# Kernel tuning notes

Hardware: AMD Instinct MI355X
Metric: run time of the kernel (lower is better)

## Reference

```python
import jax, jax.numpy as jnp
import numpy as np


def setup_inputs() -> dict:
    key = jax.random.key(0)
    k1, k2, k3, k4 = jax.random.split(key, 4)
    B, I, O, N, T = 4096, 512, 64, 32, 4
    E = N * T
    x = jax.random.normal(k1, (B, I), dtype=jnp.float32)
    dst_state = jax.random.uniform(k2, (B, N), dtype=jnp.float32)
    type_state = jax.random.uniform(k3, (B, T), dtype=jnp.float32)
    # orthogonal init with gain=0.01 approximated by small random weights; bias=0
    W = jax.random.normal(k4, (E, I, O), dtype=jnp.float32) * 0.01
    b = jnp.zeros((E, O), dtype=jnp.float32)
    return {"x": x, "dst_state": dst_state, "type_state": type_state, "W": W, "b": b}


def reference(x, dst_state, type_state, W, b):
    # gating weights: outer product of dst_state [B,N] and type_state [B,T],
    # flattened to [B, E] with E = N*T (row-major, matching torch view)
    B = x.shape[0]
    g = (dst_state[:, :, None] * type_state[:, None, :]).reshape(B, -1)  # [B,E]
    # per-expert linear then gated sum over experts, fused via einsum
    logits = jnp.einsum("bi,eio,be->bo", x, W, g) + jnp.einsum("be,eo->bo", g, b)
    # torch.distributions.Categorical(logits=...) normalizes logits
    return jax.nn.log_softmax(logits, axis=-1)
```

## Files before the change

kernel.cpp:

```cpp
#include <hip/hip_runtime.h>
#include <hip/hip_bf16.h>

typedef __bf16 bf16x8 __attribute__((ext_vector_type(8)));
typedef float  f32x4  __attribute__((ext_vector_type(4)));

#define B_SZ 4096
#define I_SZ 512
#define O_SZ 64
#define E_SZ 128
#define BM   256
#define G_EXP 8
#define EG_N  16
#define MT_N  16

__global__ void prep_xg(const float* __restrict__ x, __bf16* __restrict__ xb,
                        const float* __restrict__ ds, const float* __restrict__ ts,
                        float* __restrict__ gT) {
  int i = blockIdx.x * 256 + threadIdx.x;
  float4 v = ((const float4*)x)[i];
  union { __bf16 h[4]; ushort4 u4; } pk;
  pk.h[0] = (__bf16)v.x; pk.h[1] = (__bf16)v.y;
  pk.h[2] = (__bf16)v.z; pk.h[3] = (__bf16)v.w;
  ((ushort4*)xb)[i] = pk.u4;
  int e = i >> 12, b = i & 4095;
  gT[i] = ds[b * 32 + (e >> 2)] * ts[b * 4 + (e & 3)];
}

__global__ void prep_w(const float* __restrict__ W, __bf16* __restrict__ wt) {
  __shared__ __bf16 tile[64][66];
  int e  = blockIdx.x >> 3;
  int it = blockIdx.x & 7;
  const float* src = W + (size_t)e * I_SZ * O_SZ + (size_t)it * 64 * O_SZ;
  #pragma unroll
  for (int s = 0; s < 16; ++s) {
    int idx = s * 256 + threadIdx.x;
    int r = idx >> 6, o = idx & 63;
    tile[o][r] = (__bf16)src[idx];
  }
  __syncthreads();
  __bf16* dst = wt + (size_t)e * O_SZ * I_SZ + it * 64;
  #pragma unroll
  for (int s = 0; s < 4; ++s) {
    int idx = s * 256 + threadIdx.x;
    int o = idx >> 4, c = (idx & 15) << 2;
    union { __bf16 h[4]; ushort4 u4; } q;
    q.h[0] = tile[o][c + 0]; q.h[1] = tile[o][c + 1];
    q.h[2] = tile[o][c + 2]; q.h[3] = tile[o][c + 3];
    *(ushort4*)&dst[(size_t)o * I_SZ + c] = q.u4;
  }
}

__global__ __launch_bounds__(512, 2)
void mtc_gemm(const __bf16* __restrict__ xb, const __bf16* __restrict__ wt,
              const float* __restrict__ gT, const float* __restrict__ bias,
              float* __restrict__ partials) {
  __shared__ __align__(16) __bf16 wsh[2][8][64 * 64];
  __shared__ float gsh[G_EXP][BM];
  __shared__ float bsh[G_EXP][O_SZ];

  const int tid  = threadIdx.x;
  const int wave = tid >> 6;
  const int lane = tid & 63;

  int bid = (int)blockIdx.x;
  bid = (bid & 7) * 32 + (bid >> 3);
  const int mtile = bid & 15;
  const int eg    = bid >> 4;
  const int row0  = mtile * BM;
  const int e0    = eg * G_EXP;

  auto stage = [&](int sbuf, int e) {
    const __bf16* wsrc = wt + (size_t)(e0 + e) * O_SZ * I_SZ;
    int o = tid >> 3, p = tid & 7;
    int sl = p ^ (o & 7);
    #pragma unroll
    for (int kc = 0; kc < 8; ++kc) {
      __builtin_amdgcn_global_load_lds(
          (const __attribute__((address_space(1))) void*)(wsrc + (size_t)o * I_SZ + kc * 64 + sl * 8),
          (__attribute__((address_space(3))) void*)(&wsh[sbuf][kc][wave * 512]),
          16, 0, 0);
    }
  };

  stage(0, 0);

  for (int idx = tid; idx < G_EXP * BM; idx += 512)
    gsh[idx >> 8][idx & 255] =
        gT[(size_t)(e0 + (idx >> 8)) * B_SZ + row0 + (idx & 255)];

  bsh[tid >> 6][tid & 63] = bias[(size_t)e0 * O_SZ + tid];

  bf16x8 af[2][16];
  {
    const __bf16* xr = xb + (size_t)(row0 + wave * 32 + (lane & 15)) * I_SZ
                          + (lane >> 4) * 8;
    #pragma unroll
    for (int mf = 0; mf < 2; ++mf)
      #pragma unroll
      for (int j = 0; j < 16; ++j)
        af[mf][j] = *(const bf16x8*)(xr + mf * 16 * I_SZ + j * 32);
  }

  __syncthreads();

  f32x4 logits[2][4] = {};
  int buf = 0;
  for (int e = 0; e < G_EXP; ++e) {
    if (e < G_EXP - 1) {
      stage(buf ^ 1, e + 1);
      asm volatile("s_waitcnt vmcnt(8)" ::: "memory");
    } else {
      asm volatile("s_waitcnt vmcnt(0)" ::: "memory");
    }
    __builtin_amdgcn_s_barrier();

    float bv[4];
    #pragma unroll
    for (int nf = 0; nf < 4; ++nf)
      bv[nf] = bsh[e][nf * 16 + (lane & 15)];
    f32x4 acc[2][4];
    #pragma unroll
    for (int mf = 0; mf < 2; ++mf)
      #pragma unroll
      for (int nf = 0; nf < 4; ++nf)
        acc[mf][nf] = (f32x4){bv[nf], bv[nf], bv[nf], bv[nf]};

    __builtin_amdgcn_s_setprio(1);
    #pragma unroll
    for (int j = 0; j < 16; ++j) {
      const __bf16* wb = &wsh[buf][j >> 1][0];
      bf16x8 bfr[4];
      #pragma unroll
      for (int nf = 0; nf < 4; ++nf) {
        int o  = nf * 16 + (lane & 15);
        int q  = (j & 1) * 4 + (lane >> 4);
        int ph = q ^ (o & 7);
        bfr[nf] = *(const bf16x8*)(wb + o * 64 + ph * 8);
      }
      #pragma unroll
      for (int nf = 0; nf < 4; ++nf)
        #pragma unroll
        for (int mf = 0; mf < 2; ++mf)
          acc[mf][nf] = __builtin_amdgcn_mfma_f32_16x16x32_bf16(
              af[mf][j], bfr[nf], acc[mf][nf], 0, 0, 0);
    }
    __builtin_amdgcn_s_setprio(0);

    f32x4 gq[2];
    #pragma unroll
    for (int mf = 0; mf < 2; ++mf)
      gq[mf] = *(const f32x4*)&gsh[e][wave * 32 + mf * 16 + (lane >> 4) * 4];
    #pragma unroll
    for (int mf = 0; mf < 2; ++mf)
      #pragma unroll
      for (int nf = 0; nf < 4; ++nf)
        #pragma unroll
        for (int rg = 0; rg < 4; ++rg)
          logits[mf][nf][rg] += gq[mf][rg] * acc[mf][nf][rg];

    __builtin_amdgcn_s_barrier();
    buf ^= 1;
  }

  float* pout = partials + (size_t)eg * B_SZ * O_SZ + (size_t)row0 * O_SZ;
  #pragma unroll
  for (int mf = 0; mf < 2; ++mf)
    #pragma unroll
    for (int nf = 0; nf < 4; ++nf)
      #pragma unroll
      for (int rg = 0; rg < 4; ++rg) {
        int r = wave * 32 + mf * 16 + ((lane >> 4) << 2) + rg;
        int o = nf * 16 + (lane & 15);
        pout[(size_t)r * O_SZ + o] = logits[mf][nf][rg];
      }
}

__global__ __launch_bounds__(256)
void mtc_reduce(const float* __restrict__ partials, float* __restrict__ out) {
  int wave = threadIdx.x >> 6, lane = threadIdx.x & 63;
  int r = blockIdx.x * 4 + wave;
  float s = 0.f;
  #pragma unroll
  for (int k = 0; k < EG_N; ++k)
    s += partials[(size_t)k * B_SZ * O_SZ + (size_t)r * O_SZ + lane];
  float m = s;
  #pragma unroll
  for (int off = 32; off; off >>= 1) m = fmaxf(m, __shfl_xor(m, off));
  float ex = expf(s - m), sum = ex;
  #pragma unroll
  for (int off = 32; off; off >>= 1) sum += __shfl_xor(sum, off);
  out[(size_t)r * O_SZ + lane] = s - m - logf(sum);
}

extern "C" void kernel_launch(void* const* d_in, const int* in_sizes, int n_in,
                              void* d_out, int out_size, void* d_ws, size_t ws_size,
                              hipStream_t stream) {
  const float* x    = (const float*)d_in[0];
  const float* ds   = (const float*)d_in[1];
  const float* ts   = (const float*)d_in[2];
  const float* W    = (const float*)d_in[3];
  const float* bias = (const float*)d_in[4];
  float* out = (float*)d_out;

  char* w = (char*)d_ws;
  __bf16* xb      = (__bf16*)(w);
  __bf16* wt      = (__bf16*)(w + (4ull  << 20));
  float*  gT      = (float*) (w + (12ull << 20));
  float*  parts   = (float*) (w + (14ull << 20));

  prep_xg   <<<2048, 256, 0, stream>>>(x, xb, ds, ts, gT);
  prep_w    <<<1024, 256, 0, stream>>>(W, wt);
  mtc_gemm  <<< 256, 512, 0, stream>>>(xb, wt, gT, bias, parts);
  mtc_reduce<<<1024, 256, 0, stream>>>(parts, out);
}
```

Baseline: 58.19 us.

## Split K across wave pairs to halve LDS B-fragment reads in MoE GEMM

```diff
diff --git a/kernel.cpp b/kernel.cpp
--- a/kernel.cpp
+++ b/kernel.cpp
@@ -61,6 +61,8 @@
   const int tid  = threadIdx.x;
   const int wave = tid >> 6;
   const int lane = tid & 63;
+  const int rg   = wave >> 1;
+  const int kh   = wave & 1;
 
   int bid = (int)blockIdx.x;
   bid = (bid & 7) * 32 + (bid >> 3);
@@ -77,7 +79,7 @@
     for (int kc = 0; kc < 8; ++kc) {
       __builtin_amdgcn_global_load_lds(
           (const __attribute__((address_space(1))) void*)(wsrc + (size_t)o * I_SZ + kc * 64 + sl * 8),
-          (__attribute__((address_space(3))) void*)(&wsh[sbuf][kc][wave * 512]),
+          (__attribute__((address_space(3))) void*)(&wsh[sbuf][kc][(tid >> 6) * 512]),
           16, 0, 0);
     }
   };
@@ -90,20 +92,20 @@
 
   bsh[tid >> 6][tid & 63] = bias[(size_t)e0 * O_SZ + tid];
 
-  bf16x8 af[2][16];
+  bf16x8 af[4][8];
   {
-    const __bf16* xr = xb + (size_t)(row0 + wave * 32 + (lane & 15)) * I_SZ
-                          + (lane >> 4) * 8;
-    #pragma unroll
-    for (int mf = 0; mf < 2; ++mf)
-      #pragma unroll
-      for (int j = 0; j < 16; ++j)
+    const __bf16* xr = xb + (size_t)(row0 + rg * 64 + (lane & 15)) * I_SZ
+                          + kh * 256 + (lane >> 4) * 8;
+    #pragma unroll
+    for (int mf = 0; mf < 4; ++mf)
+      #pragma unroll
+      for (int j = 0; j < 8; ++j)
         af[mf][j] = *(const bf16x8*)(xr + mf * 16 * I_SZ + j * 32);
   }
 
   __syncthreads();
 
-  f32x4 logits[2][4] = {};
+  f32x4 logits[4][4] = {};
   int buf = 0;
   for (int e = 0; e < G_EXP; ++e) {
     if (e < G_EXP - 1) {
@@ -114,65 +116,66 @@
     }
     __builtin_amdgcn_s_barrier();
 
-    float bv[4];
-    #pragma unroll
-    for (int nf = 0; nf < 4; ++nf)
-      bv[nf] = bsh[e][nf * 16 + (lane & 15)];
-    f32x4 acc[2][4];
-    #pragma unroll
-    for (int mf = 0; mf < 2; ++mf)
-      #pragma unroll
-      for (int nf = 0; nf < 4; ++nf)
-        acc[mf][nf] = (f32x4){bv[nf], bv[nf], bv[nf], bv[nf]};
-
-    __builtin_amdgcn_s_setprio(1);
-    #pragma unroll
-    for (int j = 0; j < 16; ++j) {
-      const __bf16* wb = &wsh[buf][j >> 1][0];
-      bf16x8 bfr[4];
-      #pragma unroll
-      for (int nf = 0; nf < 4; ++nf) {
+    #pragma unroll
+    for (int nf = 0; nf < 4; ++nf) {
+      float bv = kh ? 0.f : bsh[e][nf * 16 + (lane & 15)];
+      f32x4 acc[4];
+      #pragma unroll
+      for (int mf = 0; mf < 4; ++mf)
+        acc[mf] = (f32x4){bv, bv, bv, bv};
+
+      __builtin_amdgcn_s_setprio(1);
+      #pragma unroll
+      for (int j = 0; j < 8; ++j) {
+        const __bf16* wb = &wsh[buf][kh * 4 + (j >> 1)][0];
         int o  = nf * 16 + (lane & 15);
         int q  = (j & 1) * 4 + (lane >> 4);
         int ph = q ^ (o & 7);
-        bfr[nf] = *(const bf16x8*)(wb + o * 64 + ph * 8);
+        bf16x8 bfr = *(const bf16x8*)(wb + o * 64 + ph * 8);
+        #pragma unroll
+        for (int mf = 0; mf < 4; ++mf)
+          acc[mf] = __builtin_amdgcn_mfma_f32_16x16x32_bf16(
+              af[mf][j], bfr, acc[mf], 0, 0, 0);
       }
-      #pragma unroll
-      for (int nf = 0; nf < 4; ++nf)
+      __builtin_amdgcn_s_setprio(0);
+
+      #pragma unroll
+      for (int mf = 0; mf < 4; ++mf) {
+        f32x4 gq = *(const f32x4*)&gsh[e][rg * 64 + mf * 16 + (lane >> 4) * 4];
         #pragma unroll
-        for (int mf = 0; mf < 2; ++mf)
-          acc[mf][nf] = __builtin_amdgcn_mfma_f32_16x16x32_bf16(
-              af[mf][j], bfr[nf], acc[mf][nf], 0, 0, 0);
+        for (int rgi = 0; rgi < 4; ++rgi)
+          logits[mf][nf][rgi] += gq[rgi] * acc[mf][rgi];
+      }
     }
-    __builtin_amdgcn_s_setprio(0);
-
-    f32x4 gq[2];
-    #pragma unroll
-    for (int mf = 0; mf < 2; ++mf)
-      gq[mf] = *(const f32x4*)&gsh[e][wave * 32 + mf * 16 + (lane >> 4) * 4];
-    #pragma unroll
-    for (int mf = 0; mf < 2; ++mf)
-      #pragma unroll
-      for (int nf = 0; nf < 4; ++nf)
-        #pragma unroll
-        for (int rg = 0; rg < 4; ++rg)
-          logits[mf][nf][rg] += gq[mf][rg] * acc[mf][nf][rg];
 
     __builtin_amdgcn_s_barrier();
     buf ^= 1;
   }
 
-  float* pout = partials + (size_t)eg * B_SZ * O_SZ + (size_t)row0 * O_SZ;
-  #pragma unroll
-  for (int mf = 0; mf < 2; ++mf)
-    #pragma unroll
-    for (int nf = 0; nf < 4; ++nf)
-      #pragma unroll
-      for (int rg = 0; rg < 4; ++rg) {
-        int r = wave * 32 + mf * 16 + ((lane >> 4) << 2) + rg;
-        int o = nf * 16 + (lane & 15);
-        pout[(size_t)r * O_SZ + o] = logits[mf][nf][rg];
+  float* exch = (float*)&wsh[0][0][0];
+  if (kh) {
+    #pragma unroll
+    for (int mf = 0; mf < 4; ++mf)
+      #pragma unroll
+      for (int nf = 0; nf < 4; ++nf)
+        *(f32x4*)&exch[rg * 4096 + (mf * 4 + nf) * 256 + lane * 4] = logits[mf][nf];
+  }
+  __syncthreads();
+  if (!kh) {
+    float* pout = partials + (size_t)eg * B_SZ * O_SZ + (size_t)row0 * O_SZ;
+    #pragma unroll
+    for (int mf = 0; mf < 4; ++mf)
+      #pragma unroll
+      for (int nf = 0; nf < 4; ++nf) {
+        f32x4 other = *(const f32x4*)&exch[rg * 4096 + (mf * 4 + nf) * 256 + lane * 4];
+        #pragma unroll
+        for (int rgi = 0; rgi < 4; ++rgi) {
+          int r = rg * 64 + mf * 16 + ((lane >> 4) << 2) + rgi;
+          int o = nf * 16 + (lane & 15);
+          pout[(size_t)r * O_SZ + o] = logits[mf][nf][rgi] + other[rgi];
+        }
       }
+  }
 }
 
 __global__ __launch_bounds__(256)
```

Measured after the change: 124.0 us. 113% more time.

## Halve GEMM row tile and split K staging to double block count

Applied to the files above, without the earlier changes.

```diff
diff --git a/kernel.cpp b/kernel.cpp
--- a/kernel.cpp
+++ b/kernel.cpp
@@ -8,10 +8,10 @@
 #define I_SZ 512
 #define O_SZ 64
 #define E_SZ 128
-#define BM   256
+#define BM   128
 #define G_EXP 8
 #define EG_N  16
-#define MT_N  16
+#define MT_N  32
 
 __global__ void prep_xg(const float* __restrict__ x, __bf16* __restrict__ xb,
                         const float* __restrict__ ds, const float* __restrict__ ts,
@@ -50,11 +50,11 @@
   }
 }
 
-__global__ __launch_bounds__(512, 2)
+__global__ __launch_bounds__(256, 2)
 void mtc_gemm(const __bf16* __restrict__ xb, const __bf16* __restrict__ wt,
               const float* __restrict__ gT, const float* __restrict__ bias,
               float* __restrict__ partials) {
-  __shared__ __align__(16) __bf16 wsh[2][8][64 * 64];
+  __shared__ __align__(16) __bf16 wsh[2][4][64 * 64];
   __shared__ float gsh[G_EXP][BM];
   __shared__ float bsh[G_EXP][O_SZ];
 
@@ -63,32 +63,33 @@
   const int lane = tid & 63;
 
   int bid = (int)blockIdx.x;
-  bid = (bid & 7) * 32 + (bid >> 3);
-  const int mtile = bid & 15;
-  const int eg    = bid >> 4;
+  bid = (bid & 7) * 64 + (bid >> 3);
+  const int mtile = bid & 31;
+  const int eg    = bid >> 5;
   const int row0  = mtile * BM;
   const int e0    = eg * G_EXP;
 
-  auto stage = [&](int sbuf, int e) {
-    const __bf16* wsrc = wt + (size_t)(e0 + e) * O_SZ * I_SZ;
-    int o = tid >> 3, p = tid & 7;
-    int sl = p ^ (o & 7);
-    #pragma unroll
-    for (int kc = 0; kc < 8; ++kc) {
+  auto stage = [&](int sbuf, int e, int kh) {
+    const __bf16* wsrc = wt + (size_t)(e0 + e) * O_SZ * I_SZ + kh * 256;
+    #pragma unroll
+    for (int d = 0; d < 8; ++d) {
+      int o  = (d & 1) * 32 + (tid >> 3);
+      int sl = (tid & 7) ^ (o & 7);
       __builtin_amdgcn_global_load_lds(
-          (const __attribute__((address_space(1))) void*)(wsrc + (size_t)o * I_SZ + kc * 64 + sl * 8),
-          (__attribute__((address_space(3))) void*)(&wsh[sbuf][kc][wave * 512]),
+          (const __attribute__((address_space(1))) void*)(wsrc + (size_t)o * I_SZ + (d >> 1) * 64 + sl * 8),
+          (__attribute__((address_space(3))) void*)(&wsh[sbuf][d >> 1][(d & 1) * 2048 + tid * 8]),
           16, 0, 0);
     }
   };
 
-  stage(0, 0);
-
-  for (int idx = tid; idx < G_EXP * BM; idx += 512)
-    gsh[idx >> 8][idx & 255] =
-        gT[(size_t)(e0 + (idx >> 8)) * B_SZ + row0 + (idx & 255)];
-
-  bsh[tid >> 6][tid & 63] = bias[(size_t)e0 * O_SZ + tid];
+  stage(0, 0, 0);
+
+  for (int idx = tid; idx < G_EXP * BM; idx += 256)
+    gsh[idx >> 7][idx & 127] =
+        gT[(size_t)(e0 + (idx >> 7)) * B_SZ + row0 + (idx & 127)];
+
+  for (int idx = tid; idx < G_EXP * O_SZ; idx += 256)
+    bsh[idx >> 6][idx & 63] = bias[(size_t)e0 * O_SZ + idx];
 
   bf16x8 af[2][16];
   {
@@ -97,66 +98,72 @@
     #pragma unroll
     for (int mf = 0; mf < 2; ++mf)
       #pragma unroll
-      for (int j = 0; j < 16; ++j)
-        af[mf][j] = *(const bf16x8*)(xr + mf * 16 * I_SZ + j * 32);
+      for (int jg = 0; jg < 16; ++jg)
+        af[mf][jg] = *(const bf16x8*)(xr + mf * 16 * I_SZ + jg * 32);
   }
 
   __syncthreads();
 
   f32x4 logits[2][4] = {};
+  f32x4 acc[2][4];
   int buf = 0;
-  for (int e = 0; e < G_EXP; ++e) {
-    if (e < G_EXP - 1) {
-      stage(buf ^ 1, e + 1);
+  for (int ph = 0; ph < 2 * G_EXP; ++ph) {
+    const int e  = ph >> 1;
+    const int kh = ph & 1;
+    if (ph < 2 * G_EXP - 1) {
+      stage(buf ^ 1, (ph + 1) >> 1, (ph + 1) & 1);
       asm volatile("s_waitcnt vmcnt(8)" ::: "memory");
     } else {
       asm volatile("s_waitcnt vmcnt(0)" ::: "memory");
     }
     __builtin_amdgcn_s_barrier();
 
-    float bv[4];
-    #pragma unroll
-    for (int nf = 0; nf < 4; ++nf)
-      bv[nf] = bsh[e][nf * 16 + (lane & 15)];
-    f32x4 acc[2][4];
-    #pragma unroll
-    for (int mf = 0; mf < 2; ++mf)
+    if (!kh) {
+      float bv[4];
       #pragma unroll
       for (int nf = 0; nf < 4; ++nf)
-        acc[mf][nf] = (f32x4){bv[nf], bv[nf], bv[nf], bv[nf]};
+        bv[nf] = bsh[e][nf * 16 + (lane & 15)];
+      #pragma unroll
+      for (int mf = 0; mf < 2; ++mf)
+        #pragma unroll
+        for (int nf = 0; nf < 4; ++nf)
+          acc[mf][nf] = (f32x4){bv[nf], bv[nf], bv[nf], bv[nf]};
+    }
 
     __builtin_amdgcn_s_setprio(1);
     #pragma unroll
-    for (int j = 0; j < 16; ++j) {
+    for (int j = 0; j < 8; ++j) {
       const __bf16* wb = &wsh[buf][j >> 1][0];
       bf16x8 bfr[4];
       #pragma unroll
       for (int nf = 0; nf < 4; ++nf) {
         int o  = nf * 16 + (lane & 15);
         int q  = (j & 1) * 4 + (lane >> 4);
-        int ph = q ^ (o & 7);
-        bfr[nf] = *(const bf16x8*)(wb + o * 64 + ph * 8);
+        int phs = q ^ (o & 7);
+        bfr[nf] = *(const bf16x8*)(wb + o * 64 + phs * 8);
       }
       #pragma unroll
       for (int nf = 0; nf < 4; ++nf)
         #pragma unroll
         for (int mf = 0; mf < 2; ++mf)
           acc[mf][nf] = __builtin_amdgcn_mfma_f32_16x16x32_bf16(
-              af[mf][j], bfr[nf], acc[mf][nf], 0, 0, 0);
+              af[mf][kh * 8 + j], bfr[nf], acc[mf][nf], 0, 0, 0);
     }
     __builtin_amdgcn_s_setprio(0);
 
-    f32x4 gq[2];
-    #pragma unroll
-    for (int mf = 0; mf < 2; ++mf)
-      gq[mf] = *(const f32x4*)&gsh[e][wave * 32 + mf * 16 + (lane >> 4) * 4];
-    #pragma unroll
-    for (int mf = 0; mf < 2; ++mf)
-      #pragma unroll
-      for (int nf = 0; nf < 4; ++nf)
+    if (kh) {
+      f32x4 gq[2];
+      #pragma unroll
+      for (int mf = 0; mf < 2; ++mf)
+        gq[mf] = *(const f32x4*)&gsh[e][wave * 32 + mf * 16 + (lane >> 4) * 4];
+      #pragma unroll
+      for (int mf = 0; mf < 2; ++mf)
         #pragma unroll
-        for (int rg = 0; rg < 4; ++rg)
-          logits[mf][nf][rg] += gq[mf][rg] * acc[mf][nf][rg];
+        for (int nf = 0; nf < 4; ++nf)
+          #pragma unroll
+          for (int rg = 0; rg < 4; ++rg)
+            logits[mf][nf][rg] += gq[mf][rg] * acc[mf][nf][rg];
+    }
 
     __builtin_amdgcn_s_barrier();
     buf ^= 1;
@@ -210,6 +217,6 @@
 
   prep_xg   <<<2048, 256, 0, stream>>>(x, xb, ds, ts, gT);
   prep_w    <<<1024, 256, 0, stream>>>(W, wt);
-  mtc_gemm  <<< 256, 512, 0, stream>>>(xb, wt, gT, bias, parts);
+  mtc_gemm  <<< 512, 256, 0, stream>>>(xb, wt, gT, bias, parts);
   mtc_reduce<<<1024, 256, 0, stream>>>(parts, out);
 }
```

Result: slower. 117.5 us (+102.0%).

## Fuse x conversion and gate computation into GEMM; store partials in bf16

Applied to the files above, without the earlier changes.

```diff
diff --git a/kernel.cpp b/kernel.cpp
--- a/kernel.cpp
+++ b/kernel.cpp
@@ -13,19 +13,6 @@
 #define EG_N  16
 #define MT_N  16
 
-__global__ void prep_xg(const float* __restrict__ x, __bf16* __restrict__ xb,
-                        const float* __restrict__ ds, const float* __restrict__ ts,
-                        float* __restrict__ gT) {
-  int i = blockIdx.x * 256 + threadIdx.x;
-  float4 v = ((const float4*)x)[i];
-  union { __bf16 h[4]; ushort4 u4; } pk;
-  pk.h[0] = (__bf16)v.x; pk.h[1] = (__bf16)v.y;
-  pk.h[2] = (__bf16)v.z; pk.h[3] = (__bf16)v.w;
-  ((ushort4*)xb)[i] = pk.u4;
-  int e = i >> 12, b = i & 4095;
-  gT[i] = ds[b * 32 + (e >> 2)] * ts[b * 4 + (e & 3)];
-}
-
 __global__ void prep_w(const float* __restrict__ W, __bf16* __restrict__ wt) {
   __shared__ __bf16 tile[64][66];
   int e  = blockIdx.x >> 3;
@@ -51,9 +38,9 @@
 }
 
 __global__ __launch_bounds__(512, 2)
-void mtc_gemm(const __bf16* __restrict__ xb, const __bf16* __restrict__ wt,
-              const float* __restrict__ gT, const float* __restrict__ bias,
-              float* __restrict__ partials) {
+void mtc_gemm(const float* __restrict__ x, const __bf16* __restrict__ wt,
+              const float* __restrict__ ds, const float* __restrict__ ts,
+              const float* __restrict__ bias, __bf16* __restrict__ partials) {
   __shared__ __align__(16) __bf16 wsh[2][8][64 * 64];
   __shared__ float gsh[G_EXP][BM];
   __shared__ float bsh[G_EXP][O_SZ];
@@ -84,21 +71,31 @@
 
   stage(0, 0);
 
-  for (int idx = tid; idx < G_EXP * BM; idx += 512)
-    gsh[idx >> 8][idx & 255] =
-        gT[(size_t)(e0 + (idx >> 8)) * B_SZ + row0 + (idx & 255)];
+  for (int idx = tid; idx < G_EXP * BM; idx += 512) {
+    int k = idx >> 8, r = idx & 255;
+    gsh[k][r] = ds[(size_t)(row0 + r) * 32 + ((e0 + k) >> 2)]
+              * ts[(size_t)(row0 + r) * 4 + (k & 3)];
+  }
 
   bsh[tid >> 6][tid & 63] = bias[(size_t)e0 * O_SZ + tid];
 
   bf16x8 af[2][16];
   {
-    const __bf16* xr = xb + (size_t)(row0 + wave * 32 + (lane & 15)) * I_SZ
-                          + (lane >> 4) * 8;
-    #pragma unroll
-    for (int mf = 0; mf < 2; ++mf)
-      #pragma unroll
-      for (int j = 0; j < 16; ++j)
-        af[mf][j] = *(const bf16x8*)(xr + mf * 16 * I_SZ + j * 32);
+    const float* xr = x + (size_t)(row0 + wave * 32 + (lane & 15)) * I_SZ
+                        + (lane >> 4) * 8;
+    #pragma unroll
+    for (int mf = 0; mf < 2; ++mf)
+      #pragma unroll
+      for (int j = 0; j < 16; ++j) {
+        f32x4 a = *(const f32x4*)(xr + mf * 16 * I_SZ + j * 32);
+        f32x4 b = *(const f32x4*)(xr + mf * 16 * I_SZ + j * 32 + 4);
+        bf16x8 v;
+        v[0] = (__bf16)a[0]; v[1] = (__bf16)a[1];
+        v[2] = (__bf16)a[2]; v[3] = (__bf16)a[3];
+        v[4] = (__bf16)b[0]; v[5] = (__bf16)b[1];
+        v[6] = (__bf16)b[2]; v[7] = (__bf16)b[3];
+        af[mf][j] = v;
+      }
   }
 
   __syncthreads();
@@ -162,7 +159,7 @@
     buf ^= 1;
   }
 
-  float* pout = partials + (size_t)eg * B_SZ * O_SZ + (size_t)row0 * O_SZ;
+  __bf16* pout = partials + (size_t)eg * B_SZ * O_SZ + (size_t)row0 * O_SZ;
   #pragma unroll
   for (int mf = 0; mf < 2; ++mf)
     #pragma unroll
@@ -171,18 +168,18 @@
       for (int rg = 0; rg < 4; ++rg) {
         int r = wave * 32 + mf * 16 + ((lane >> 4) << 2) + rg;
         int o = nf * 16 + (lane & 15);
-        pout[(size_t)r * O_SZ + o] = logits[mf][nf][rg];
+        pout[(size_t)r * O_SZ + o] = (__bf16)logits[mf][nf][rg];
       }
 }
 
 __global__ __launch_bounds__(256)
-void mtc_reduce(const float* __restrict__ partials, float* __restrict__ out) {
+void mtc_reduce(const __bf16* __restrict__ partials, float* __restrict__ out) {
   int wave = threadIdx.x >> 6, lane = threadIdx.x & 63;
   int r = blockIdx.x * 4 + wave;
   float s = 0.f;
   #pragma unroll
   for (int k = 0; k < EG_N; ++k)
-    s += partials[(size_t)k * B_SZ * O_SZ + (size_t)r * O_SZ + lane];
+    s += (float)partials[(size_t)k * B_SZ * O_SZ + (size_t)r * O_SZ + lane];
   float m = s;
   #pragma unroll
   for (int off = 32; off; off >>= 1) m = fmaxf(m, __shfl_xor(m, off));
@@ -203,13 +200,10 @@
   float* out = (float*)d_out;
 
   char* w = (char*)d_ws;
-  __bf16* xb      = (__bf16*)(w);
-  __bf16* wt      = (__bf16*)(w + (4ull  << 20));
-  float*  gT      = (float*) (w + (12ull << 20));
-  float*  parts   = (float*) (w + (14ull << 20));
-
-  prep_xg   <<<2048, 256, 0, stream>>>(x, xb, ds, ts, gT);
+  __bf16* wt      = (__bf16*)(w);
+  __bf16* parts   = (__bf16*)(w + (8ull << 20));
+
   prep_w    <<<1024, 256, 0, stream>>>(W, wt);
-  mtc_gemm  <<< 256, 512, 0, stream>>>(xb, wt, gT, bias, parts);
+  mtc_gemm  <<< 256, 512, 0, stream>>>(x, wt, ds, ts, bias, parts);
   mtc_reduce<<<1024, 256, 0, stream>>>(parts, out);
 }
```

Measured after the change: 60.80 us. 1.04x slower.
